# Kernel tuning notes

Hardware: AMD Instinct MI355X
Metric: run time of the kernel (lower is better)

Reference implementation:

```python
import jax, jax.numpy as jnp
import numpy as np

N_NODES = 100000
D = 128
N_EDGES = 640000


def _spmm(edge_index, w, x, n):
    # out[i] = sum over edges (i<-j): w * x[j]
    src, dst = edge_index[0], edge_index[1]
    return jax.ops.segment_sum(w[:, None] * x[dst], src, num_segments=n)


def setup_inputs() -> dict:
    key = jax.random.key(0)
    ks = jax.random.split(key, 8)
    inp = {
        "index_vectors": jax.random.normal(ks[0], (N_NODES, D), dtype=jnp.float32),
        "edge_index1": jax.random.randint(ks[1], (2, N_EDGES), 0, N_NODES, dtype=jnp.int64),
        "w1": jnp.ones((N_EDGES,), dtype=jnp.float32),
        "edge_index2": jax.random.randint(ks[2], (2, N_EDGES), 0, N_NODES, dtype=jnp.int64),
        "w2": jnp.ones((N_EDGES,), dtype=jnp.float32),
        "edge_index3": jax.random.randint(ks[3], (2, N_EDGES), 0, N_NODES, dtype=jnp.int64),
        "w3": jnp.ones((N_EDGES,), dtype=jnp.float32),
        "zeroth": jax.random.uniform(ks[4], (1, 1), dtype=jnp.float32),
        "fst": jax.random.uniform(ks[5], (1, 1), dtype=jnp.float32),
        "snd": jax.random.uniform(ks[6], (1, 1), dtype=jnp.float32),
        "trd": jax.random.uniform(ks[7], (1, 1), dtype=jnp.float32),
    }
    return inp


def reference(index_vectors, edge_index1, w1, edge_index2, w2, edge_index3, w3,
              zeroth, fst, snd, trd):
    n = index_vectors.shape[0]
    # hop-1 context: A @ x
    fst_ctx = _spmm(edge_index1, w1, index_vectors, n)
    # hop-2 context: A^2 @ roll(x, 1, axis=1)   (permute_vecs=True)
    snd_ctx = _spmm(edge_index2, w2, jnp.roll(index_vectors, 1, axis=1), n)
    # hop-3 context: A^3 @ roll(x, 2, axis=1)
    trd_ctx = _spmm(edge_index3, w3, jnp.roll(index_vectors, 2, axis=1), n)

    # relu-normalized scalar order weights (get_orders)
    r0, r1, r2, r3 = (jax.nn.relu(zeroth), jax.nn.relu(fst),
                      jax.nn.relu(snd), jax.nn.relu(trd))
    tot = r0 + r1 + r2 + r3 + 1e-6
    r0, r1, r2, r3 = r0 / tot, r1 / tot, r2 / tot, r3 / tot

    # use_sign=False -> plain weighted combination
    return r0 * index_vectors + r1 * fst_ctx + r2 * snd_ctx + r3 * trd_ctx
```

## Files before the change

kernel.cpp:

```cpp
#include <hip/hip_runtime.h>

#define N_NODES 100000
#define D 128
#define N_EDGES 640000
#define TOT_EDGES (3 * N_EDGES)

#define NB   256
#define NPB  391
#define BCAP 9216
#define OVF_CAP 16384
#define EPB  3072
#define BINA_BLOCKS (TOT_EDGES / EPB)
#define EPT  (EPB / 256)

#define WS_OVFCNT 0
#define WS_BCUR   64
#define WS_BBASE  16448
#define WS_BNUM   17472
#define WS_OVF    18496
#define WS_TMP    280640
#define WS_FREC   19155008
#define WS_OFFS   34515008
#define WS_XB     34915016
#define WS_TOTAL_FAST 60515016

__device__ __forceinline__ void load_r(const float* z0, const float* z1,
                                       const float* z2, const float* z3,
                                       float& r0, float& r1, float& r2, float& r3) {
    r0 = fmaxf(z0[0], 0.0f);
    r1 = fmaxf(z1[0], 0.0f);
    r2 = fmaxf(z2[0], 0.0f);
    r3 = fmaxf(z3[0], 0.0f);
    float inv = 1.0f / (r0 + r1 + r2 + r3 + 1e-6f);
    r0 *= inv; r1 *= inv; r2 *= inv; r3 *= inv;
}

__device__ __forceinline__ unsigned short bf16rn(float f) {
    unsigned int u = __float_as_uint(f);
    u += 0x7FFFu + ((u >> 16) & 1u);
    return (unsigned short)(u >> 16);
}

__global__ void cast_kernel(const float* __restrict__ x, ushort* __restrict__ xb) {
    int i = blockIdx.x * 256 + threadIdx.x;
    if (i >= N_NODES * D / 4) return;
    float4 v = ((const float4*)x)[i];
    ushort4 h;
    h.x = bf16rn(v.x); h.y = bf16rn(v.y); h.z = bf16rn(v.z); h.w = bf16rn(v.w);
    ((ushort4*)xb)[i] = h;
}

__global__ void binA_kernel(const int* __restrict__ ei1, const float* __restrict__ w1,
                            const int* __restrict__ ei2, const float* __restrict__ w2,
                            const int* __restrict__ ei3, const float* __restrict__ w3,
                            const float* __restrict__ z0, const float* __restrict__ z1,
                            const float* __restrict__ z2, const float* __restrict__ z3,
                            int* __restrict__ bcur, int* __restrict__ ovf_count,
                            int4* __restrict__ ovf, int2* __restrict__ tmp) {
    __shared__ int hist[NB];
    __shared__ int base[NB];
    int t = threadIdx.x;
    hist[t] = 0;
    __syncthreads();

    int e0 = blockIdx.x * EPB;
    int rank[EPT];
    int bkt[EPT];

    for (int k = 0; k < EPT; ++k) {
        int e = e0 + t + k * 256;
        int set = e / N_EDGES;
        int idx = e - set * N_EDGES;
        const int* ei = (set == 0) ? ei1 : (set == 1) ? ei2 : ei3;
        int src = ei[idx];
        int b = src / NPB;
        bkt[k]  = b;
        rank[k] = atomicAdd(&hist[b], 1);
    }
    __syncthreads();

    {
        int h = hist[t];
        base[t] = h ? atomicAdd(&bcur[t * 16], h) : 0;
    }
    __syncthreads();

    float r0, r1, r2, r3;
    load_r(z0, z1, z2, z3, r0, r1, r2, r3);

    for (int k = 0; k < EPT; ++k) {
        int e = e0 + t + k * 256;
        int set = e / N_EDGES;
        int idx = e - set * N_EDGES;
        const int* ei;  const float* w;
        if      (set == 0) { ei = ei1; w = w1; }
        else if (set == 1) { ei = ei2; w = w2; }
        else               { ei = ei3; w = w3; }
        int src = ei[idx];
        int dst = ei[N_EDGES + idx];
        float rk = (set == 0) ? r1 : (set == 1) ? r2 : r3;
        float scale = rk * w[idx];
        int b = bkt[k];
        int local = src - b * NPB;
        int pos = base[b] + rank[k];
        int rx = dst | (set << 17) | (local << 19);
        if (pos < BCAP) {
            tmp[(size_t)b * BCAP + pos] = make_int2(rx, __float_as_int(scale));
        } else {
            int o = atomicAdd(ovf_count, 1);
            if (o < OVF_CAP) ovf[o] = make_int4(src, dst | (set << 17),
                                                __float_as_int(scale), 0);
        }
    }
}

__global__ void scanB_kernel(const int* __restrict__ bcur,
                             int* __restrict__ bbase, int* __restrict__ bnum,
                             int* __restrict__ offsets) {
    __shared__ int s[NB];
    int t = threadIdx.x;
    int n = bcur[t * 16];
    if (n > BCAP) n = BCAP;
    bnum[t] = n;
    s[t] = n;
    __syncthreads();
    for (int off = 1; off < NB; off <<= 1) {
        int v = (t >= off) ? s[t - off] : 0;
        __syncthreads();
        s[t] += v;
        __syncthreads();
    }
    bbase[t] = s[t] - n;
    if (t == NB - 1) offsets[N_NODES] = s[t];
}

__global__ void binB_kernel(const int2* __restrict__ tmp,
                            const int* __restrict__ bbase, const int* __restrict__ bnum,
                            int2* __restrict__ frecs, int* __restrict__ offsets) {
    __shared__ int d[512];
    __shared__ int s[512];
    __shared__ int cur[NPB];
    int b = blockIdx.x;
    int t = threadIdx.x;
    int n = bnum[b];
    int gbase = bbase[b];

    d[t] = 0; d[t + 256] = 0;
    __syncthreads();
    for (int i = t; i < n; i += 256) {
        int rx = tmp[(size_t)b * BCAP + i].x;
        atomicAdd(&d[(rx >> 19) & 0x1FF], 1);
    }
    __syncthreads();
    s[t] = d[t]; s[t + 256] = d[t + 256];
    __syncthreads();
    for (int off = 1; off < 512; off <<= 1) {
        int v0 = (t       >= off) ? s[t       - off] : 0;
        int v1 = (t + 256 >= off) ? s[t + 256 - off] : 0;
        __syncthreads();
        s[t] += v0; s[t + 256] += v1;
        __syncthreads();
    }
    int node0 = b * NPB;
    for (int l = t; l < NPB; l += 256) {
        int excl = s[l] - d[l];
        cur[l] = excl;
        int node = node0 + l;
        if (node < N_NODES) offsets[node] = gbase + excl;
    }
    __syncthreads();
    for (int i = t; i < n; i += 256) {
        int2 rec = tmp[(size_t)b * BCAP + i];
        int pos = atomicAdd(&cur[(rec.x >> 19) & 0x1FF], 1);
        frecs[gbase + pos] = make_int2(rec.x & 0x7FFFF, rec.y);
    }
}

__global__ void gatherb_kernel(const float* __restrict__ x,
                               const ushort* __restrict__ xb,
                               const int* __restrict__ offsets,
                               const int2* __restrict__ recs,
                               const float* __restrict__ z0, const float* __restrict__ z1,
                               const float* __restrict__ z2, const float* __restrict__ z3,
                               float* __restrict__ out) {
    int wid  = (blockIdx.x * blockDim.x + threadIdx.x) >> 6;
    int lane = threadIdx.x & 63;
    if (wid >= N_NODES) return;

    float r0, r1, r2, r3;
    load_r(z0, z1, z2, z3, r0, r1, r2, r3);

    float2 xv = ((const float2*)(x + (size_t)wid * D))[lane];

    int beg = offsets[wid];
    int end = offsets[wid + 1];
    int count = end - beg;
    int cnt64 = (count < 64) ? count : 64;

    int2 myrec = make_int2(0, 0);
    if (lane < cnt64) myrec = recs[beg + lane];

    float2 a0 = {0.f, 0.f}, a1 = {0.f, 0.f}, a2 = {0.f, 0.f};

    int j = 0;
    for (; j + 3 < cnt64; j += 4) {
        int rxa = __shfl(myrec.x, j),     rya = __shfl(myrec.y, j);
        int rxb = __shfl(myrec.x, j + 1), ryb = __shfl(myrec.y, j + 1);
        int rxc = __shfl(myrec.x, j + 2), ryc = __shfl(myrec.y, j + 2);
        int rxd = __shfl(myrec.x, j + 3), ryd = __shfl(myrec.y, j + 3);
        unsigned int va = ((const unsigned int*)(xb + (size_t)(rxa & 0x1FFFF) * D))[lane];
        unsigned int vb = ((const unsigned int*)(xb + (size_t)(rxb & 0x1FFFF) * D))[lane];
        unsigned int vc = ((const unsigned int*)(xb + (size_t)(rxc & 0x1FFFF) * D))[lane];
        unsigned int vd = ((const unsigned int*)(xb + (size_t)(rxd & 0x1FFFF) * D))[lane];
        int sha = (rxa >> 17) & 3, shb = (rxb >> 17) & 3;
        int shc = (rxc >> 17) & 3, shd = (rxd >> 17) & 3;
        float sca = __int_as_float(rya), scb = __int_as_float(ryb);
        float scc = __int_as_float(ryc), scd = __int_as_float(ryd);
        float ax = __uint_as_float(va << 16), ay = __uint_as_float(va & 0xFFFF0000u);
        float bx = __uint_as_float(vb << 16), by = __uint_as_float(vb & 0xFFFF0000u);
        float cx = __uint_as_float(vc << 16), cy = __uint_as_float(vc & 0xFFFF0000u);
        float dx = __uint_as_float(vd << 16), dy = __uint_as_float(vd & 0xFFFF0000u);
        if      (sha == 0) { a0.x += sca * ax; a0.y += sca * ay; }
        else if (sha == 1) { a1.x += sca * ax; a1.y += sca * ay; }
        else               { a2.x += sca * ax; a2.y += sca * ay; }
        if      (shb == 0) { a0.x += scb * bx; a0.y += scb * by; }
        else if (shb == 1) { a1.x += scb * bx; a1.y += scb * by; }
        else               { a2.x += scb * bx; a2.y += scb * by; }
        if      (shc == 0) { a0.x += scc * cx; a0.y += scc * cy; }
        else if (shc == 1) { a1.x += scc * cx; a1.y += scc * cy; }
        else               { a2.x += scc * cx; a2.y += scc * cy; }
        if      (shd == 0) { a0.x += scd * dx; a0.y += scd * dy; }
        else if (shd == 1) { a1.x += scd * dx; a1.y += scd * dy; }
        else               { a2.x += scd * dx; a2.y += scd * dy; }
    }
    for (; j < cnt64; ++j) {
        int rx = __shfl(myrec.x, j), ry = __shfl(myrec.y, j);
        unsigned int vv = ((const unsigned int*)(xb + (size_t)(rx & 0x1FFFF) * D))[lane];
        int sh = (rx >> 17) & 3;
        float sc = __int_as_float(ry);
        float vx = __uint_as_float(vv << 16), vy = __uint_as_float(vv & 0xFFFF0000u);
        if      (sh == 0) { a0.x += sc * vx; a0.y += sc * vy; }
        else if (sh == 1) { a1.x += sc * vx; a1.y += sc * vy; }
        else               { a2.x += sc * vx; a2.y += sc * vy; }
    }
    for (int q = 64; q < count; ++q) {
        int2 rec = recs[beg + q];
        unsigned int vv = ((const unsigned int*)(xb + (size_t)(rec.x & 0x1FFFF) * D))[lane];
        int sh = (rec.x >> 17) & 3;
        float sc = __int_as_float(rec.y);
        float vx = __uint_as_float(vv << 16), vy = __uint_as_float(vv & 0xFFFF0000u);
        if      (sh == 0) { a0.x += sc * vx; a0.y += sc * vy; }
        else if (sh == 1) { a1.x += sc * vx; a1.y += sc * vy; }
        else               { a2.x += sc * vx; a2.y += sc * vy; }
    }

    int prev = (lane + 63) & 63;
    float r1y = __shfl(a1.y, prev);
    float r2x = __shfl(a2.x, prev);
    float r2y = __shfl(a2.y, prev);
    float2 o;
    o.x = r0 * xv.x + a0.x + r1y  + r2x;
    o.y = r0 * xv.y + a0.y + a1.x + r2y;
    ((float2*)(out + (size_t)wid * D))[lane] = o;
}

__global__ void ovf_kernel(const float* __restrict__ x,
                           const int* __restrict__ ovf_count,
                           const int4* __restrict__ ovf,
                           float* __restrict__ out) {
    int total_waves = (gridDim.x * blockDim.x) >> 6;
    int gw   = (blockIdx.x * blockDim.x + threadIdx.x) >> 6;
    int lane = threadIdx.x & 63;
    int n = *ovf_count;
    if (n > OVF_CAP) n = OVF_CAP;
    for (int r = gw; r < n; r += total_waves) {
        int4 rec = ovf[r];
        int src = rec.x;
        int dst = rec.y & 0x1FFFF;
        int sh  = (rec.y >> 17) & 3;
        float sc = __int_as_float(rec.z);
        const float* xr = x + (size_t)dst * D;
        float* orow = out + (size_t)src * D;
        int c0 = 2 * lane, c1 = 2 * lane + 1;
        atomicAdd(&orow[c0], sc * xr[(c0 - sh) & 127]);
        atomicAdd(&orow[c1], sc * xr[(c1 - sh) & 127]);
    }
}

#define SCAN_BLOCKS ((N_NODES + 255) / 256)
#define WS_COUNTS   0
#define WS_OFFSETS  400000
#define WS_CURSORS  800008
#define WS_BSUM     1200008
#define WS_BPRE     1201576
#define WS_RECS     1203144
#define WS_NEEDED_MID (WS_RECS + (size_t)TOT_EDGES * 8)

__global__ void hist_kernel(const int* __restrict__ ei1, const int* __restrict__ ei2,
                            const int* __restrict__ ei3, int* __restrict__ counts) {
    int e = blockIdx.x * blockDim.x + threadIdx.x;
    if (e >= TOT_EDGES) return;
    int set = e / N_EDGES;
    int idx = e - set * N_EDGES;
    const int* ei = (set == 0) ? ei1 : (set == 1) ? ei2 : ei3;
    atomicAdd(&counts[ei[idx]], 1);
}

__global__ void scan1_kernel(const int* __restrict__ counts,
                             int* __restrict__ offsets, int* __restrict__ bsum) {
    __shared__ int s[256];
    int t = threadIdx.x;
    int i = blockIdx.x * 256 + t;
    int v = (i < N_NODES) ? counts[i] : 0;
    s[t] = v;
    __syncthreads();
    for (int off = 1; off < 256; off <<= 1) {
        int u = (t >= off) ? s[t - off] : 0;
        __syncthreads();
        s[t] += u;
        __syncthreads();
    }
    if (i < N_NODES) offsets[i] = s[t] - v;
    if (t == 255) bsum[blockIdx.x] = s[255];
}

__global__ void scan2_kernel(const int* __restrict__ bsum, int* __restrict__ bpre) {
    __shared__ int s[512];
    int t = threadIdx.x;
    int v = (t < SCAN_BLOCKS) ? bsum[t] : 0;
    s[t] = v;
    __syncthreads();
    for (int off = 1; off < 512; off <<= 1) {
        int u = (t >= off) ? s[t - off] : 0;
        __syncthreads();
        s[t] += u;
        __syncthreads();
    }
    if (t < SCAN_BLOCKS) bpre[t] = s[t] - v;
}

__global__ void scan3_kernel(int* __restrict__ offsets, const int* __restrict__ bpre,
                             int* __restrict__ cursors) {
    int i = blockIdx.x * 256 + threadIdx.x;
    if (i < N_NODES) {
        int v = offsets[i] + bpre[blockIdx.x];
        offsets[i] = v;
        cursors[i] = v;
    }
    if (i == 0) offsets[N_NODES] = TOT_EDGES;
}

__global__ void fill_kernel(const int* __restrict__ ei1, const float* __restrict__ w1,
                            const int* __restrict__ ei2, const float* __restrict__ w2,
                            const int* __restrict__ ei3, const float* __restrict__ w3,
                            const float* __restrict__ z0, const float* __restrict__ z1,
                            const float* __restrict__ z2, const float* __restrict__ z3,
                            int* __restrict__ cursors, int2* __restrict__ recs) {
    int e = blockIdx.x * blockDim.x + threadIdx.x;
    if (e >= TOT_EDGES) return;
    int set = e / N_EDGES;
    int idx = e - set * N_EDGES;
    const int* ei;  const float* w;
    if      (set == 0) { ei = ei1; w = w1; }
    else if (set == 1) { ei = ei2; w = w2; }
    else               { ei = ei3; w = w3; }
    float r0, r1, r2, r3;
    load_r(z0, z1, z2, z3, r0, r1, r2, r3);
    float rk = (set == 0) ? r1 : (set == 1) ? r2 : r3;
    int src = ei[idx];
    int dst = ei[N_EDGES + idx];
    float scale = rk * w[idx];
    int pos = atomicAdd(&cursors[src], 1);
    recs[pos] = make_int2(dst | (set << 17), __float_as_int(scale));
}

__global__ void gatherd_kernel(const float* __restrict__ x,
                               const int* __restrict__ offsets,
                               const int2* __restrict__ recs,
                               const float* __restrict__ z0, const float* __restrict__ z1,
                               const float* __restrict__ z2, const float* __restrict__ z3,
                               float* __restrict__ out) {
    int wid  = (blockIdx.x * blockDim.x + threadIdx.x) >> 6;
    int lane = threadIdx.x & 63;
    if (wid >= N_NODES) return;
    float r0, r1, r2, r3;
    load_r(z0, z1, z2, z3, r0, r1, r2, r3);
    float2 xv = ((const float2*)(x + (size_t)wid * D))[lane];
    int beg = offsets[wid];
    int end = offsets[wid + 1];
    float2 a0 = {0.f, 0.f}, a1 = {0.f, 0.f}, a2 = {0.f, 0.f};
    for (int j = beg; j < end; ++j) {
        int2 rec = recs[j];
        float2 v = ((const float2*)(x + (size_t)(rec.x & 0x1FFFF) * D))[lane];
        int sh = (rec.x >> 17) & 3;
        float sc = __int_as_float(rec.y);
        if      (sh == 0) { a0.x += sc * v.x; a0.y += sc * v.y; }
        else if (sh == 1) { a1.x += sc * v.x; a1.y += sc * v.y; }
        else               { a2.x += sc * v.x; a2.y += sc * v.y; }
    }
    int prev = (lane + 63) & 63;
    float r1y = __shfl(a1.y, prev);
    float r2x = __shfl(a2.x, prev);
    float r2y = __shfl(a2.y, prev);
    float2 o;
    o.x = r0 * xv.x + a0.x + r1y  + r2x;
    o.y = r0 * xv.y + a0.y + a1.x + r2y;
    ((float2*)(out + (size_t)wid * D))[lane] = o;
}

extern "C" void kernel_launch(void* const* d_in, const int* in_sizes, int n_in,
                              void* d_out, int out_size, void* d_ws, size_t ws_size,
                              hipStream_t stream) {
    const float* x   = (const float*)d_in[0];
    const int*   ei1 = (const int*)  d_in[1];
    const float* w1  = (const float*)d_in[2];
    const int*   ei2 = (const int*)  d_in[3];
    const float* w2  = (const float*)d_in[4];
    const int*   ei3 = (const int*)  d_in[5];
    const float* w3  = (const float*)d_in[6];
    const float* z0  = (const float*)d_in[7];
    const float* z1  = (const float*)d_in[8];
    const float* z2  = (const float*)d_in[9];
    const float* z3  = (const float*)d_in[10];
    float* out = (float*)d_out;
    char* wsc = (char*)d_ws;

    if (ws_size >= WS_TOTAL_FAST) {
        int*    ovf_count = (int*)   (wsc + WS_OVFCNT);
        int*    bcur      = (int*)   (wsc + WS_BCUR);
        int*    bbase     = (int*)   (wsc + WS_BBASE);
        int*    bnum      = (int*)   (wsc + WS_BNUM);
        int4*   ovf       = (int4*)  (wsc + WS_OVF);
        int2*   tmp       = (int2*)  (wsc + WS_TMP);
        int2*   frecs     = (int2*)  (wsc + WS_FREC);
        int*    offsets   = (int*)   (wsc + WS_OFFS);
        ushort* xb        = (ushort*)(wsc + WS_XB);

        hipMemsetAsync(wsc, 0, WS_BBASE, stream);
        cast_kernel<<<(N_NODES * D / 4 + 255) / 256, 256, 0, stream>>>(x, xb);
        binA_kernel<<<BINA_BLOCKS, 256, 0, stream>>>(ei1, w1, ei2, w2, ei3, w3,
                                                     z0, z1, z2, z3,
                                                     bcur, ovf_count, ovf, tmp);
        scanB_kernel<<<1, NB, 0, stream>>>(bcur, bbase, bnum, offsets);
        binB_kernel<<<NB, 256, 0, stream>>>(tmp, bbase, bnum, frecs, offsets);
        gatherb_kernel<<<(N_NODES * 64 + 255) / 256, 256, 0, stream>>>(x, xb, offsets,
                                                                       frecs, z0, z1, z2, z3,
                                                                       out);
        ovf_kernel<<<128, 256, 0, stream>>>(x, ovf_count, ovf, out);
    } else {
        int*  counts  = (int*) (wsc + WS_COUNTS);
        int*  offsets = (int*) (wsc + WS_OFFSETS);
        int*  cursors = (int*) (wsc + WS_CURSORS);
        int*  bsum    = (int*) (wsc + WS_BSUM);
        int*  bpre    = (int*) (wsc + WS_BPRE);
        int2* recs    = (int2*)(wsc + WS_RECS);

        hipMemsetAsync(counts, 0, N_NODES * sizeof(int), stream);
        hist_kernel<<<TOT_EDGES / 256, 256, 0, stream>>>(ei1, ei2, ei3, counts);
        scan1_kernel<<<SCAN_BLOCKS, 256, 0, stream>>>(counts, offsets, bsum);
        scan2_kernel<<<1, 512, 0, stream>>>(bsum, bpre);
        scan3_kernel<<<SCAN_BLOCKS, 256, 0, stream>>>(offsets, bpre, cursors);
        fill_kernel<<<TOT_EDGES / 256, 256, 0, stream>>>(ei1, w1, ei2, w2, ei3, w3,
                                                         z0, z1, z2, z3, cursors, recs);
        gatherd_kernel<<<(N_NODES * 64 + 255) / 256, 256, 0, stream>>>(x, offsets, recs,
                                                                       z0, z1, z2, z3, out);
    }
}
```

Before: 300.9 us.

## Gather four edges per wave with 16-byte row loads and set-sorted records

The gather kernel now processes four edges per wave iteration: each quarter-wave loads one bf16 row as uint4 (16 bytes per lane) instead of the whole wave loading 4 bytes per lane per edge. Partial sums are then reduced across the quarters with xor shuffles, and 16 lanes write the output with float4 stores. binB now sorts records by a (node, set) key so edges of the same hop are contiguous, which reduces divergence in the three-way accumulate branch. binA reads src, dst and weight once and keeps them in registers instead of reloading them in its second pass. The cost is more accumulator registers and a cross-lane reduction at the end, which may lower occupancy.

```diff
diff --git a/kernel.cpp b/kernel.cpp
--- a/kernel.cpp
+++ b/kernel.cpp
@@ -12,6 +12,7 @@
 #define EPB  3072
 #define BINA_BLOCKS (TOT_EDGES / EPB)
 #define EPT  (EPB / 256)
+#define NKEY 2048
 
 #define WS_OVFCNT 0
 #define WS_BCUR   64
@@ -63,18 +64,31 @@
     hist[t] = 0;
     __syncthreads();
 
+    float r0, r1, r2, r3;
+    load_r(z0, z1, z2, z3, r0, r1, r2, r3);
+
     int e0 = blockIdx.x * EPB;
     int rank[EPT];
     int bkt[EPT];
-
+    int rxv[EPT];
+    float scv[EPT];
+
+#pragma unroll
     for (int k = 0; k < EPT; ++k) {
         int e = e0 + t + k * 256;
         int set = e / N_EDGES;
         int idx = e - set * N_EDGES;
-        const int* ei = (set == 0) ? ei1 : (set == 1) ? ei2 : ei3;
+        const int* ei;  const float* w;  float rk;
+        if      (set == 0) { ei = ei1; w = w1; rk = r1; }
+        else if (set == 1) { ei = ei2; w = w2; rk = r2; }
+        else               { ei = ei3; w = w3; rk = r3; }
         int src = ei[idx];
+        int dst = ei[N_EDGES + idx];
         int b = src / NPB;
+        int local = src - b * NPB;
         bkt[k]  = b;
+        rxv[k]  = dst | (set << 17) | (local << 19);
+        scv[k]  = rk * w[idx];
         rank[k] = atomicAdd(&hist[b], 1);
     }
     __syncthreads();
@@ -85,31 +99,17 @@
     }
     __syncthreads();
 
-    float r0, r1, r2, r3;
-    load_r(z0, z1, z2, z3, r0, r1, r2, r3);
-
+#pragma unroll
     for (int k = 0; k < EPT; ++k) {
-        int e = e0 + t + k * 256;
-        int set = e / N_EDGES;
-        int idx = e - set * N_EDGES;
-        const int* ei;  const float* w;
-        if      (set == 0) { ei = ei1; w = w1; }
-        else if (set == 1) { ei = ei2; w = w2; }
-        else               { ei = ei3; w = w3; }
-        int src = ei[idx];
-        int dst = ei[N_EDGES + idx];
-        float rk = (set == 0) ? r1 : (set == 1) ? r2 : r3;
-        float scale = rk * w[idx];
         int b = bkt[k];
-        int local = src - b * NPB;
         int pos = base[b] + rank[k];
-        int rx = dst | (set << 17) | (local << 19);
         if (pos < BCAP) {
-            tmp[(size_t)b * BCAP + pos] = make_int2(rx, __float_as_int(scale));
+            tmp[(size_t)b * BCAP + pos] = make_int2(rxv[k], __float_as_int(scv[k]));
         } else {
             int o = atomicAdd(ovf_count, 1);
-            if (o < OVF_CAP) ovf[o] = make_int4(src, dst | (set << 17),
-                                                __float_as_int(scale), 0);
+            int src = b * NPB + ((rxv[k] >> 19) & 0x1FF);
+            if (o < OVF_CAP) ovf[o] = make_int4(src, rxv[k] & 0x7FFFF,
+                                                __float_as_int(scv[k]), 0);
         }
     }
 }
@@ -137,43 +137,89 @@
 __global__ void binB_kernel(const int2* __restrict__ tmp,
                             const int* __restrict__ bbase, const int* __restrict__ bnum,
                             int2* __restrict__ frecs, int* __restrict__ offsets) {
-    __shared__ int d[512];
-    __shared__ int s[512];
-    __shared__ int cur[NPB];
+    __shared__ int d[NKEY];
+    __shared__ int ts[256];
+    __shared__ int cur[NKEY];
     int b = blockIdx.x;
     int t = threadIdx.x;
     int n = bnum[b];
     int gbase = bbase[b];
 
-    d[t] = 0; d[t + 256] = 0;
+    for (int i = t; i < NKEY; i += 256) d[i] = 0;
     __syncthreads();
     for (int i = t; i < n; i += 256) {
         int rx = tmp[(size_t)b * BCAP + i].x;
-        atomicAdd(&d[(rx >> 19) & 0x1FF], 1);
-    }
-    __syncthreads();
-    s[t] = d[t]; s[t + 256] = d[t + 256];
-    __syncthreads();
-    for (int off = 1; off < 512; off <<= 1) {
-        int v0 = (t       >= off) ? s[t       - off] : 0;
-        int v1 = (t + 256 >= off) ? s[t + 256 - off] : 0;
-        __syncthreads();
-        s[t] += v0; s[t + 256] += v1;
-        __syncthreads();
-    }
+        int key = (((rx >> 19) & 0x1FF) << 2) | ((rx >> 17) & 3);
+        atomicAdd(&d[key], 1);
+    }
+    __syncthreads();
+
+    int loc[8];
+    int tot = 0;
+#pragma unroll
+    for (int k = 0; k < 8; ++k) { loc[k] = tot; tot += d[8 * t + k]; }
+    ts[t] = tot;
+    __syncthreads();
+    for (int off = 1; off < 256; off <<= 1) {
+        int v = (t >= off) ? ts[t - off] : 0;
+        __syncthreads();
+        ts[t] += v;
+        __syncthreads();
+    }
+    int tbase = ts[t] - tot;
+#pragma unroll
+    for (int k = 0; k < 8; ++k) cur[8 * t + k] = tbase + loc[k];
+    __syncthreads();
+
     int node0 = b * NPB;
     for (int l = t; l < NPB; l += 256) {
-        int excl = s[l] - d[l];
-        cur[l] = excl;
         int node = node0 + l;
-        if (node < N_NODES) offsets[node] = gbase + excl;
-    }
-    __syncthreads();
+        if (node < N_NODES) offsets[node] = gbase + cur[l << 2];
+    }
+    __syncthreads();
+
     for (int i = t; i < n; i += 256) {
         int2 rec = tmp[(size_t)b * BCAP + i];
-        int pos = atomicAdd(&cur[(rec.x >> 19) & 0x1FF], 1);
+        int key = (((rec.x >> 19) & 0x1FF) << 2) | ((rec.x >> 17) & 3);
+        int pos = atomicAdd(&cur[key], 1);
         frecs[gbase + pos] = make_int2(rec.x & 0x7FFFF, rec.y);
     }
+}
+
+__device__ __forceinline__ void accum4(int rx, int ry, int l16,
+                                       const ushort* __restrict__ xb,
+                                       float4& a0lo, float4& a0hi,
+                                       float4& a1lo, float4& a1hi,
+                                       float4& a2lo, float4& a2hi) {
+    const uint4* rowp = (const uint4*)(xb + (size_t)(rx & 0x1FFFF) * D);
+    uint4 v = rowp[l16];
+    int sh = (rx >> 17) & 3;
+    float sc = __int_as_float(ry);
+    float p0 = __uint_as_float(v.x << 16);
+    float p1 = __uint_as_float(v.x & 0xFFFF0000u);
+    float p2 = __uint_as_float(v.y << 16);
+    float p3 = __uint_as_float(v.y & 0xFFFF0000u);
+    float p4 = __uint_as_float(v.z << 16);
+    float p5 = __uint_as_float(v.z & 0xFFFF0000u);
+    float p6 = __uint_as_float(v.w << 16);
+    float p7 = __uint_as_float(v.w & 0xFFFF0000u);
+    if (sh == 0) {
+        a0lo.x += sc * p0; a0lo.y += sc * p1; a0lo.z += sc * p2; a0lo.w += sc * p3;
+        a0hi.x += sc * p4; a0hi.y += sc * p5; a0hi.z += sc * p6; a0hi.w += sc * p7;
+    } else if (sh == 1) {
+        a1lo.x += sc * p0; a1lo.y += sc * p1; a1lo.z += sc * p2; a1lo.w += sc * p3;
+        a1hi.x += sc * p4; a1hi.y += sc * p5; a1hi.z += sc * p6; a1hi.w += sc * p7;
+    } else {
+        a2lo.x += sc * p0; a2lo.y += sc * p1; a2lo.z += sc * p2; a2lo.w += sc * p3;
+        a2hi.x += sc * p4; a2hi.y += sc * p5; a2hi.z += sc * p6; a2hi.w += sc * p7;
+    }
+}
+
+__device__ __forceinline__ void red4(float4& v) {
+    v.x += __shfl_xor(v.x, 16); v.y += __shfl_xor(v.y, 16);
+    v.z += __shfl_xor(v.z, 16); v.w += __shfl_xor(v.w, 16);
+    v.x += __shfl_xor(v.x, 32); v.y += __shfl_xor(v.y, 32);
+    v.z += __shfl_xor(v.z, 32); v.w += __shfl_xor(v.w, 32);
 }
 
 __global__ void gatherb_kernel(const float* __restrict__ x,
@@ -190,7 +236,8 @@
     float r0, r1, r2, r3;
     load_r(z0, z1, z2, z3, r0, r1, r2, r3);
 
-    float2 xv = ((const float2*)(x + (size_t)wid * D))[lane];
+    int qt  = lane >> 4;
+    int l16 = lane & 15;
 
     int beg = offsets[wid];
     int end = offsets[wid + 1];
@@ -200,68 +247,47 @@
     int2 myrec = make_int2(0, 0);
     if (lane < cnt64) myrec = recs[beg + lane];
 
-    float2 a0 = {0.f, 0.f}, a1 = {0.f, 0.f}, a2 = {0.f, 0.f};
-
-    int j = 0;
-    for (; j + 3 < cnt64; j += 4) {
-        int rxa = __shfl(myrec.x, j),     rya = __shfl(myrec.y, j);
-        int rxb = __shfl(myrec.x, j + 1), ryb = __shfl(myrec.y, j + 1);
-        int rxc = __shfl(myrec.x, j + 2), ryc = __shfl(myrec.y, j + 2);
-        int rxd = __shfl(myrec.x, j + 3), ryd = __shfl(myrec.y, j + 3);
-        unsigned int va = ((const unsigned int*)(xb + (size_t)(rxa & 0x1FFFF) * D))[lane];
-        unsigned int vb = ((const unsigned int*)(xb + (size_t)(rxb & 0x1FFFF) * D))[lane];
-        unsigned int vc = ((const unsigned int*)(xb + (size_t)(rxc & 0x1FFFF) * D))[lane];
-        unsigned int vd = ((const unsigned int*)(xb + (size_t)(rxd & 0x1FFFF) * D))[lane];
-        int sha = (rxa >> 17) & 3, shb = (rxb >> 17) & 3;
-        int shc = (rxc >> 17) & 3, shd = (rxd >> 17) & 3;
-        float sca = __int_as_float(rya), scb = __int_as_float(ryb);
-        float scc = __int_as_float(ryc), scd = __int_as_float(ryd);
-        float ax = __uint_as_float(va << 16), ay = __uint_as_float(va & 0xFFFF0000u);
-        float bx = __uint_as_float(vb << 16), by = __uint_as_float(vb & 0xFFFF0000u);
-        float cx = __uint_as_float(vc << 16), cy = __uint_as_float(vc & 0xFFFF0000u);
-        float dx = __uint_as_float(vd << 16), dy = __uint_as_float(vd & 0xFFFF0000u);
-        if      (sha == 0) { a0.x += sca * ax; a0.y += sca * ay; }
-        else if (sha == 1) { a1.x += sca * ax; a1.y += sca * ay; }
-        else               { a2.x += sca * ax; a2.y += sca * ay; }
-        if      (shb == 0) { a0.x += scb * bx; a0.y += scb * by; }
-        else if (shb == 1) { a1.x += scb * bx; a1.y += scb * by; }
-        else               { a2.x += scb * bx; a2.y += scb * by; }
-        if      (shc == 0) { a0.x += scc * cx; a0.y += scc * cy; }
-        else if (shc == 1) { a1.x += scc * cx; a1.y += scc * cy; }
-        else               { a2.x += scc * cx; a2.y += scc * cy; }
-        if      (shd == 0) { a0.x += scd * dx; a0.y += scd * dy; }
-        else if (shd == 1) { a1.x += scd * dx; a1.y += scd * dy; }
-        else               { a2.x += scd * dx; a2.y += scd * dy; }
-    }
-    for (; j < cnt64; ++j) {
-        int rx = __shfl(myrec.x, j), ry = __shfl(myrec.y, j);
-        unsigned int vv = ((const unsigned int*)(xb + (size_t)(rx & 0x1FFFF) * D))[lane];
-        int sh = (rx >> 17) & 3;
-        float sc = __int_as_float(ry);
-        float vx = __uint_as_float(vv << 16), vy = __uint_as_float(vv & 0xFFFF0000u);
-        if      (sh == 0) { a0.x += sc * vx; a0.y += sc * vy; }
-        else if (sh == 1) { a1.x += sc * vx; a1.y += sc * vy; }
-        else               { a2.x += sc * vx; a2.y += sc * vy; }
-    }
-    for (int q = 64; q < count; ++q) {
-        int2 rec = recs[beg + q];
-        unsigned int vv = ((const unsigned int*)(xb + (size_t)(rec.x & 0x1FFFF) * D))[lane];
-        int sh = (rec.x >> 17) & 3;
-        float sc = __int_as_float(rec.y);
-        float vx = __uint_as_float(vv << 16), vy = __uint_as_float(vv & 0xFFFF0000u);
-        if      (sh == 0) { a0.x += sc * vx; a0.y += sc * vy; }
-        else if (sh == 1) { a1.x += sc * vx; a1.y += sc * vy; }
-        else               { a2.x += sc * vx; a2.y += sc * vy; }
-    }
-
-    int prev = (lane + 63) & 63;
-    float r1y = __shfl(a1.y, prev);
-    float r2x = __shfl(a2.x, prev);
-    float r2y = __shfl(a2.y, prev);
-    float2 o;
-    o.x = r0 * xv.x + a0.x + r1y  + r2x;
-    o.y = r0 * xv.y + a0.y + a1.x + r2y;
-    ((float2*)(out + (size_t)wid * D))[lane] = o;
+    float4 a0lo = {0.f,0.f,0.f,0.f}, a0hi = {0.f,0.f,0.f,0.f};
+    float4 a1lo = {0.f,0.f,0.f,0.f}, a1hi = {0.f,0.f,0.f,0.f};
+    float4 a2lo = {0.f,0.f,0.f,0.f}, a2hi = {0.f,0.f,0.f,0.f};
+
+    for (int j = 0; j < cnt64; j += 4) {
+        int srcl = j + qt;
+        int rx = __shfl(myrec.x, srcl);
+        int ry = __shfl(myrec.y, srcl);
+        accum4(rx, ry, l16, xb, a0lo, a0hi, a1lo, a1hi, a2lo, a2hi);
+    }
+    for (int q = 64; q < count; q += 4) {
+        int qq = q + qt;
+        int rx = 0, ry = 0;
+        if (qq < count) { int2 rec = recs[beg + qq]; rx = rec.x; ry = rec.y; }
+        accum4(rx, ry, l16, xb, a0lo, a0hi, a1lo, a1hi, a2lo, a2hi);
+    }
+
+    red4(a0lo); red4(a0hi); red4(a1lo); red4(a1hi); red4(a2lo); red4(a2hi);
+
+    int prev = (l16 + 15) & 15;
+    float a1p7 = __shfl(a1hi.w, prev);
+    float a2p6 = __shfl(a2hi.z, prev);
+    float a2p7 = __shfl(a2hi.w, prev);
+
+    if (lane < 16) {
+        const float4* xr = (const float4*)(x + (size_t)wid * D);
+        float4 xlo = xr[2 * l16];
+        float4 xhi = xr[2 * l16 + 1];
+        float4 olo, ohi;
+        olo.x = r0 * xlo.x + a0lo.x + a1p7   + a2p6;
+        olo.y = r0 * xlo.y + a0lo.y + a1lo.x + a2p7;
+        olo.z = r0 * xlo.z + a0lo.z + a1lo.y + a2lo.x;
+        olo.w = r0 * xlo.w + a0lo.w + a1lo.z + a2lo.y;
+        ohi.x = r0 * xhi.x + a0hi.x + a1lo.w + a2lo.z;
+        ohi.y = r0 * xhi.y + a0hi.y + a1hi.x + a2lo.w;
+        ohi.z = r0 * xhi.z + a0hi.z + a1hi.y + a2hi.x;
+        ohi.w = r0 * xhi.w + a0hi.w + a1hi.z + a2hi.y;
+        float4* op = (float4*)(out + (size_t)wid * D);
+        op[2 * l16]     = olo;
+        op[2 * l16 + 1] = ohi;
+    }
 }
 
 __global__ void ovf_kernel(const float* __restrict__ x,
```

After: 581.9 us. 93.3% more time.
